# Optimization experiments

Hardware: AMD Instinct MI355X
Metric: run time of the kernel (lower is better)

The kernel has to match this reference:

```python
import jax, jax.numpy as jnp
import numpy as np

NUM_BREAKPOINTS = 100  # module default
IMG_SHAPE = (1, 1, 4096, 8192)  # B must be 1: PWL(num_channels=1) sees (C*H*W, B)


def setup_inputs() -> dict:
    key = jax.random.key(0)
    k1, k2, k3, k4 = jax.random.split(key, 4)
    x = jax.random.uniform(k1, IMG_SHAPE, dtype=jnp.float32)
    # torchpwl.PWL parameters (num_channels=1): breakpoint x-positions, per-segment
    # slopes, and bias (function value at the leftmost breakpoint).
    x_positions = jax.random.uniform(k2, (1, NUM_BREAKPOINTS), dtype=jnp.float32)
    slopes = 1.0 + 0.1 * jax.random.normal(k3, (1, NUM_BREAKPOINTS), dtype=jnp.float32)
    biases = 0.05 * jax.random.normal(k4, (1,), dtype=jnp.float32)
    return {"x": x, "x_positions": x_positions, "slopes": slopes, "biases": biases}


def _pwl(x_flat, x_positions, slopes, biases):
    # Sloped piecewise-linear function (torchpwl.BaseSlopedPWL math), 1 channel.
    # x_flat: (N,), x_positions/slopes: (1, K), biases: (1,)
    K = x_positions.shape[1]
    sorted_x = jnp.sort(x_positions, axis=1)                     # (1, K)
    skips = jnp.roll(sorted_x, -1, axis=1) - sorted_x            # last entry never used
    cumsums = jnp.cumsum(skips * slopes, axis=1)[:, :-1]         # (1, K-1)
    betas = jnp.concatenate([biases[:, None], biases[:, None] + cumsums], axis=1)  # (1, K)
    # segment index: (# breakpoints <= x) clamped to [1, K], minus 1
    idx = jnp.clip(jnp.searchsorted(sorted_x[0], x_flat, side="right"), 1, K) - 1
    return betas[0, idx] + (x_flat - sorted_x[0, idx]) * slopes[0, idx]


def reference(x, x_positions, slopes, biases):
    # forward: flatten -> PWL -> clip(0,1) -> reshape (original returns [out])
    y = _pwl(x.reshape(-1), x_positions, slopes, biases)
    return jnp.clip(y, 0.0, 1.0).reshape(x.shape)
```

## Files before the change

kernel.cpp:

```cpp
#include <hip/hip_runtime.h>

#define K  100
#define NB 1024

typedef float fvec4 __attribute__((ext_vector_type(4)));

__global__ __launch_bounds__(1024) void pwl_setup_kernel(
    const float* __restrict__ xp, const float* __restrict__ sl,
    const float* __restrict__ bias, float2* __restrict__ bab_g,
    float* __restrict__ sx_g, float2* __restrict__ ab_g) {
  __shared__ float s_pos[K];
  __shared__ float s_slope[K];
  __shared__ float s_sorted[K];
  __shared__ float s_a[K];
  __shared__ float s_b[K];
  __shared__ unsigned short s_cnt[NB + 1];
  const int t = threadIdx.x;

  if (t < K) { s_pos[t] = xp[t]; s_slope[t] = sl[t]; }
  __syncthreads();

  if (t < K) {
    float v = s_pos[t];
    int r = 0;
    for (int j = 0; j < K; ++j) {
      float u = s_pos[j];
      r += ((u < v) || (u == v && j < t)) ? 1 : 0;
    }
    s_sorted[r] = v;
  }
  __syncthreads();

  if (t == 0) {
    float acc = bias[0];
    for (int i = 0; i < K; ++i) {
      if (i) acc += (s_sorted[i] - s_sorted[i - 1]) * s_slope[i - 1];
      float a = s_slope[i];
      s_a[i] = a;
      s_b[i] = acc - s_sorted[i] * a;
    }
  }
  __syncthreads();

  if (t < K) {
    sx_g[t] = s_sorted[t];
    ab_g[t] = make_float2(s_a[t], s_b[t]);
  }

  for (int e = t; e <= NB; e += blockDim.x) {
    float ev = (float)e * (1.0f / (float)NB);
    int c = 0;
    for (int j = 0; j < K; ++j) c += (s_sorted[j] <= ev) ? 1 : 0;
    s_cnt[e] = (unsigned short)c;
  }
  __syncthreads();

  for (int b = t; b < NB; b += blockDim.x) {
    int lo = s_cnt[b], hi = s_cnt[b + 1];
    float2 e;
    if (lo == hi) {
      int idx = min(max(lo, 1), K) - 1;
      e = make_float2(s_a[idx], s_b[idx]);
    } else {
      e.x = __builtin_huge_valf();
      e.y = __uint_as_float((unsigned)lo | ((unsigned)hi << 16));
    }
    bab_g[b] = e;
  }
}

__device__ __forceinline__ float pwl_eval(float xv,
                                          const float2* __restrict__ s_bab,
                                          const float* __restrict__ s_x,
                                          const float2* __restrict__ s_ab) {
  int b = (int)(xv * (float)NB);
  b = min(max(b, 0), NB - 1);
  float2 ab = s_bab[b];
  if (__float_as_uint(ab.x) == 0x7f800000u) {
    unsigned p = __float_as_uint(ab.y);
    int lo = (int)(p & 0xffffu);
    int hi = (int)(p >> 16);
    while (lo < hi) {
      int mid = (lo + hi) >> 1;
      if (s_x[mid] <= xv) lo = mid + 1; else hi = mid;
    }
    int idx = min(max(lo, 1), K) - 1;
    ab = s_ab[idx];
  }
  float y = fmaf(xv, ab.x, ab.y);
  return fminf(fmaxf(y, 0.0f), 1.0f);
}

__global__ __launch_bounds__(256) void pwl_main_kernel(
    const fvec4* __restrict__ x, const float2* __restrict__ bab_g,
    const float* __restrict__ sx_g, const float2* __restrict__ ab_g,
    fvec4* __restrict__ out, int n4, int n) {
  __shared__ float2 s_bab[NB];
  __shared__ float s_x[K];
  __shared__ float2 s_ab[K];
  for (int i = threadIdx.x; i < NB; i += blockDim.x) s_bab[i] = bab_g[i];
  if (threadIdx.x < K) {
    s_x[threadIdx.x] = sx_g[threadIdx.x];
    s_ab[threadIdx.x] = ab_g[threadIdx.x];
  }
  __syncthreads();

  const int stride = gridDim.x * blockDim.x;
  int i = blockIdx.x * blockDim.x + threadIdx.x;
  if (i < n4) {
    fvec4 v = __builtin_nontemporal_load(&x[i]);
    while (true) {
      int inext = i + stride;
      bool more = inext < n4;
      fvec4 vn = {};
      if (more) vn = __builtin_nontemporal_load(&x[inext]);
      fvec4 r;
      r.x = pwl_eval(v.x, s_bab, s_x, s_ab);
      r.y = pwl_eval(v.y, s_bab, s_x, s_ab);
      r.z = pwl_eval(v.z, s_bab, s_x, s_ab);
      r.w = pwl_eval(v.w, s_bab, s_x, s_ab);
      __builtin_nontemporal_store(r, &out[i]);
      if (!more) break;
      v = vn;
      i = inext;
    }
  }

  if (blockIdx.x == 0) {
    const float* xs = (const float*)x;
    float* os = (float*)out;
    for (int j = (n4 << 2) + threadIdx.x; j < n; j += blockDim.x) {
      os[j] = pwl_eval(xs[j], s_bab, s_x, s_ab);
    }
  }
}

extern "C" void kernel_launch(void* const* d_in, const int* in_sizes, int n_in,
                              void* d_out, int out_size, void* d_ws, size_t ws_size,
                              hipStream_t stream) {
  const float* x    = (const float*)d_in[0];
  const float* xp   = (const float*)d_in[1];
  const float* sl   = (const float*)d_in[2];
  const float* bias = (const float*)d_in[3];
  float* out = (float*)d_out;

  float2* bab = (float2*)d_ws;
  float* sx   = (float*)((char*)d_ws + NB * 8);
  float2* ab  = (float2*)((char*)d_ws + NB * 8 + 512);

  const int n  = in_sizes[0];
  const int n4 = n >> 2;

  pwl_setup_kernel<<<1, 1024, 0, stream>>>(xp, sl, bias, bab, sx, ab);

  const int threads = 256;
  const int blocks  = 2048;
  pwl_main_kernel<<<blocks, threads, 0, stream>>>(
      (const fvec4*)x, bab, sx, ab, (fvec4*)out, n4, n);
}
```

Measured before the change: 236.5 us.

## Parallelize setup prefix sum, linear bucket scan, and 2x unroll main loop

Replaces the serial single-thread cumulative sum in the setup kernel with a parallel Hillis-Steele scan over 128 threads. The per-element binary search inside ambiguous buckets becomes a short linear scan, since buckets rarely hold more than one or two breakpoints. The main grid-stride loop is restructured to load and evaluate two vec4s per iteration instead of software-prefetching one ahead. The changes target setup latency, branch depth and memory-level parallelism; the scan adds several barriers, and the linear search could degrade if breakpoints cluster.

```diff
diff --git a/kernel.cpp b/kernel.cpp
--- a/kernel.cpp
+++ b/kernel.cpp
@@ -14,6 +14,7 @@
   __shared__ float s_sorted[K];
   __shared__ float s_a[K];
   __shared__ float s_b[K];
+  __shared__ float s_scan[128];
   __shared__ unsigned short s_cnt[NB + 1];
   const int t = threadIdx.x;
 
@@ -31,21 +32,28 @@
   }
   __syncthreads();
 
-  if (t == 0) {
-    float acc = bias[0];
-    for (int i = 0; i < K; ++i) {
-      if (i) acc += (s_sorted[i] - s_sorted[i - 1]) * s_slope[i - 1];
-      float a = s_slope[i];
-      s_a[i] = a;
-      s_b[i] = acc - s_sorted[i] * a;
-    }
+  if (t < 128) {
+    float d = 0.0f;
+    if (t < K - 1) d = (s_sorted[t + 1] - s_sorted[t]) * s_slope[t];
+    s_scan[t] = d;
   }
   __syncthreads();
-
+  for (int off = 1; off < 128; off <<= 1) {
+    float add = 0.0f;
+    if (t < 128 && t >= off) add = s_scan[t - off];
+    __syncthreads();
+    if (t < 128) s_scan[t] += add;
+    __syncthreads();
+  }
   if (t < K) {
+    float beta = bias[0] + (t ? s_scan[t - 1] : 0.0f);
+    float a = s_slope[t];
+    s_a[t] = a;
+    s_b[t] = beta - s_sorted[t] * a;
     sx_g[t] = s_sorted[t];
-    ab_g[t] = make_float2(s_a[t], s_b[t]);
+    ab_g[t] = make_float2(a, s_b[t]);
   }
+  __syncthreads();
 
   for (int e = t; e <= NB; e += blockDim.x) {
     float ev = (float)e * (1.0f / (float)NB);
@@ -80,15 +88,23 @@
     unsigned p = __float_as_uint(ab.y);
     int lo = (int)(p & 0xffffu);
     int hi = (int)(p >> 16);
-    while (lo < hi) {
-      int mid = (lo + hi) >> 1;
-      if (s_x[mid] <= xv) lo = mid + 1; else hi = mid;
-    }
+    while (lo < hi && s_x[lo] <= xv) ++lo;
     int idx = min(max(lo, 1), K) - 1;
     ab = s_ab[idx];
   }
-  float y = fmaf(xv, ab.x, ab.y);
-  return fminf(fmaxf(y, 0.0f), 1.0f);
+  return fminf(fmaxf(fmaf(xv, ab.x, ab.y), 0.0f), 1.0f);
+}
+
+__device__ __forceinline__ fvec4 eval4(fvec4 v,
+                                       const float2* __restrict__ s_bab,
+                                       const float* __restrict__ s_x,
+                                       const float2* __restrict__ s_ab) {
+  fvec4 r;
+  r.x = pwl_eval(v.x, s_bab, s_x, s_ab);
+  r.y = pwl_eval(v.y, s_bab, s_x, s_ab);
+  r.z = pwl_eval(v.z, s_bab, s_x, s_ab);
+  r.w = pwl_eval(v.w, s_bab, s_x, s_ab);
+  return r;
 }
 
 __global__ __launch_bounds__(256) void pwl_main_kernel(
@@ -107,23 +123,17 @@
 
   const int stride = gridDim.x * blockDim.x;
   int i = blockIdx.x * blockDim.x + threadIdx.x;
+  for (; i + stride < n4; i += 2 * stride) {
+    fvec4 v0 = __builtin_nontemporal_load(&x[i]);
+    fvec4 v1 = __builtin_nontemporal_load(&x[i + stride]);
+    fvec4 r0 = eval4(v0, s_bab, s_x, s_ab);
+    fvec4 r1 = eval4(v1, s_bab, s_x, s_ab);
+    __builtin_nontemporal_store(r0, &out[i]);
+    __builtin_nontemporal_store(r1, &out[i + stride]);
+  }
   if (i < n4) {
     fvec4 v = __builtin_nontemporal_load(&x[i]);
-    while (true) {
-      int inext = i + stride;
-      bool more = inext < n4;
-      fvec4 vn = {};
-      if (more) vn = __builtin_nontemporal_load(&x[inext]);
-      fvec4 r;
-      r.x = pwl_eval(v.x, s_bab, s_x, s_ab);
-      r.y = pwl_eval(v.y, s_bab, s_x, s_ab);
-      r.z = pwl_eval(v.z, s_bab, s_x, s_ab);
-      r.w = pwl_eval(v.w, s_bab, s_x, s_ab);
-      __builtin_nontemporal_store(r, &out[i]);
-      if (!more) break;
-      v = vn;
-      i = inext;
-    }
+    __builtin_nontemporal_store(eval4(v, s_bab, s_x, s_ab), &out[i]);
   }
 
   if (blockIdx.x == 0) {
```

Result: slower. 242.4 us (+2.5%).
